# Performance work log

Hardware: AMD Instinct MI355X
Metric: run time of the kernel (lower is better)

## Reference

```python
import jax, jax.numpy as jnp
import numpy as np

BS = 4      # block_size
NH = 8      # n_heads
DH = 32     # d_head
DIN = 128   # d_input
DOUT = 128  # d_output
H = 256
W = 256
B = 2


def setup_inputs() -> dict:
    key = jax.random.key(0)
    k1, k2, k3 = jax.random.split(key, 3)
    x = jax.random.normal(k1, (B, DIN, H, W), jnp.float32)
    w_in = (jax.random.normal(k2, (3 * NH * DH, DIN), jnp.float32) * 0.05)
    b_in = jnp.full((3 * NH * DH,), 0.01, jnp.float32)
    w_out = (jax.random.normal(k3, (DOUT, NH * DH), jnp.float32) * 0.05)
    b_out = jnp.full((DOUT,), 0.01, jnp.float32)
    # positional_cross_embedding init: beta*(|x-2bs|^alpha + |y-2bs|^alpha), alpha=2, beta=1/16
    d = jnp.abs(jnp.arange(4 * BS, dtype=jnp.float32) - 2 * BS) ** 2.0
    vals = (1.0 / 16.0) * (d[:, None] + d[None, :]).reshape(-1)  # (16*bs*bs,)
    pce = jnp.tile(vals[None, :], (NH, 1)).astype(jnp.float32)
    return {"x": x, "w_in": w_in, "b_in": b_in, "w_out": w_out, "b_out": b_out, "pce": pce}


def reference(x, w_in, b_in, w_out, b_out, pce):
    Bx, din, Hx, Wx = x.shape
    hb = Wx // BS  # horizontal blocks (width axis)
    vb = Hx // BS  # vertical blocks (height axis)
    # (B, C, H, W) -> (B, W, H, C) -> (B, hb, vb, bs, bs, C)
    xt = jnp.swapaxes(x, 1, 3)
    xt = xt.reshape(Bx, hb, BS, vb, BS, din).transpose(0, 1, 3, 2, 4, 5)
    proj = xt @ w_in.T + b_in  # (B, hb, vb, bs, bs, 3*NH*DH)
    q = proj[..., :NH * DH]
    kv = proj[..., NH * DH:]
    # gather 3x3 block neighborhood via pad + concat (zero padding at borders)
    kv = jnp.pad(kv, ((0, 0), (1, 1), (1, 1), (0, 0), (0, 0), (0, 0)))
    kv = jnp.concatenate((kv[:, :-2], kv[:, 1:-1], kv[:, 2:]), axis=3)       # (B,hb,vb,3bs,bs,2C)
    kv = jnp.concatenate((kv[:, :, :-2], kv[:, :, 1:-1], kv[:, :, 2:]), axis=4)  # (B,hb,vb,3bs,3bs,2C)
    q = q.reshape(Bx, hb, vb, BS * BS, NH, DH).swapaxes(3, 4)                      # (B,hb,vb,NH,bs^2,DH)
    k = kv[..., :NH * DH].reshape(Bx, hb, vb, 9 * BS * BS, NH, DH).swapaxes(3, 4)  # (B,hb,vb,NH,9bs^2,DH)
    v = kv[..., NH * DH:].reshape(Bx, hb, vb, 9 * BS * BS, NH, DH).swapaxes(3, 4)
    # relative-position bias: gather pce per (q, kv) pair (equiv. to tensordot with one-hot masks)
    a0 = jnp.arange(BS)
    a1 = jnp.arange(3 * BS)
    net = a1[None, :] + BS - a0[:, None]  # (bs, 3bs): x_net / y_net
    idx = (4 * BS * net)[:, None, :, None] + net[None, :, None, :]  # (bs, bs, 3bs, 3bs)
    idx = idx.reshape(BS * BS, 9 * BS * BS)
    bias = pce[:, idx]  # (NH, bs^2, 9bs^2)
    # boundary cutoff: mask kv halo that falls outside the image
    ex = jnp.zeros((hb, 3 * BS), bool).at[0, :BS].set(True).at[-1, 2 * BS:].set(True)
    ey = jnp.zeros((vb, 3 * BS), bool).at[0, :BS].set(True).at[-1, 2 * BS:].set(True)
    blocked = ex[:, None, :, None] | ey[None, :, None, :]  # (hb, vb, 3bs, 3bs)
    cut = jnp.where(blocked, jnp.inf, 0.0).reshape(hb, vb, 1, 1, 9 * BS * BS)
    amask = -(bias[None, None] + cut)  # (hb, vb, NH, bs^2, 9bs^2)
    scale = 1.0 / jnp.sqrt(jnp.float32(DH))
    scores = jnp.einsum('bhvnqd,bhvnkd->bhvnqk', q, k) * scale + amask
    attn = jax.nn.softmax(scores, axis=-1)
    out = jnp.einsum('bhvnqk,bhvnkd->bhvnqd', attn, v)
    out = out.swapaxes(3, 4).reshape(Bx, hb, vb, BS * BS, NH * DH)
    out = out @ w_out.T + b_out  # (B, hb, vb, bs^2, DOUT)
    out = out.reshape(Bx, hb, vb, BS, BS, DOUT).swapaxes(2, 3).reshape(Bx, Wx, Hx, DOUT)
    return jnp.swapaxes(out, 1, 3)  # (B, DOUT, H, W)
```

## Files before the change

### kernel.cpp

```cpp
#include <hip/hip_runtime.h>


typedef __bf16 bf16x8 __attribute__((ext_vector_type(8)));
typedef float f32x4 __attribute__((ext_vector_type(4)));

__device__ __forceinline__ unsigned short f2bf(float f) {
  unsigned u = __float_as_uint(f);
  u = (u + 0x7FFFu + ((u >> 16) & 1u)) >> 16;
  return (unsigned short)u;
}

__global__ __launch_bounds__(256) void prep_w(const float* __restrict__ w_in,
                                              const float* __restrict__ w_out,
                                              unsigned short* __restrict__ wbf,
                                              unsigned short* __restrict__ wob) {
  int idx = (blockIdx.x * 256 + threadIdx.x) * 4;
  const float* src; unsigned short* dst; int off;
  if (idx < 98304) { src = w_in;  dst = wbf; off = idx; }
  else             { src = w_out; dst = wob; off = idx - 98304; }
  float4 v = *(const float4*)(src + off);
  ushort4 o;
  o.x = f2bf(v.x); o.y = f2bf(v.y); o.z = f2bf(v.z); o.w = f2bf(v.w);
  *(ushort4*)(dst + off) = o;
}

#define XS_STRIDE 136

__global__ __launch_bounds__(256) void qkv_proj(const float* __restrict__ x,
                                                const unsigned short* __restrict__ wbf,
                                                const float* __restrict__ b_in,
                                                unsigned short* __restrict__ qkv,
                                                unsigned short* __restrict__ vT) {
  __shared__ __align__(16) unsigned short xs[64 * XS_STRIDE];
  const int tid = threadIdx.x;
  const int strip = blockIdx.x, vb = blockIdx.y, b = blockIdx.z;
  const int w0 = strip * 16;
  const size_t xbase = ((size_t)b * 128) * 65536 + (size_t)(vb * 4) * 256 + (size_t)w0;

#pragma unroll
  for (int it = 0; it < 8; ++it) {
    int flat = (it * 256 + tid) * 4;
    int c = flat >> 6;
    int rem = flat & 63;
    int i1 = rem >> 4;
    int lw0 = rem & 15;
    const float4 v = *(const float4*)(x + xbase + (size_t)c * 65536 + i1 * 256 + lw0);
    float vv[4] = {v.x, v.y, v.z, v.w};
#pragma unroll
    for (int e = 0; e < 4; ++e) {
      int lw = lw0 + e;
      int u = ((lw >> 2) << 4) + ((lw & 3) << 2) + i1;
      xs[u * XS_STRIDE + c] = f2bf(vv[e]);
    }
  }
  __syncthreads();

  const int wv = tid >> 6, lane = tid & 63;
  const int l16 = lane & 15, q4 = lane >> 4;
  const size_t tile_base = ((size_t)(b * 64 + vb)) * 64 + strip * 4;

#pragma unroll 1
  for (int jt = 0; jt < 12; ++jt) {
    const int j0 = wv * 192 + jt * 16;
    bf16x8 wf[4];
    const unsigned short* wr = wbf + (size_t)(j0 + l16) * 128 + q4 * 8;
#pragma unroll
    for (int ks = 0; ks < 4; ++ks) wf[ks] = *(const bf16x8*)(wr + ks * 32);

    if (j0 < 512) {
      const float4 bi = *(const float4*)(b_in + j0 + q4 * 4);
      f32x4 acc0; acc0[0] = bi.x; acc0[1] = bi.y; acc0[2] = bi.z; acc0[3] = bi.w;
      f32x4 acc[4] = {acc0, acc0, acc0, acc0};
#pragma unroll
      for (int tt = 0; tt < 4; ++tt) {
        const unsigned short* xr = xs + (tt * 16 + l16) * XS_STRIDE + q4 * 8;
#pragma unroll
        for (int ks = 0; ks < 4; ++ks) {
          bf16x8 xf = *(const bf16x8*)(xr + ks * 32);
          acc[tt] = __builtin_amdgcn_mfma_f32_16x16x32_bf16(wf[ks], xf, acc[tt], 0, 0, 0);
        }
      }
#pragma unroll
      for (int tt = 0; tt < 4; ++tt) {
        unsigned short* dst = qkv + ((tile_base + tt) * 16 + l16) * 512 + j0 + q4 * 4;
        ushort4 o;
        o.x = f2bf(acc[tt][0]); o.y = f2bf(acc[tt][1]);
        o.z = f2bf(acc[tt][2]); o.w = f2bf(acc[tt][3]);
        *(ushort4*)dst = o;
      }
    } else {
      const float bi = b_in[j0 + l16];
      f32x4 acc0; acc0[0] = bi; acc0[1] = bi; acc0[2] = bi; acc0[3] = bi;
      f32x4 acc[4] = {acc0, acc0, acc0, acc0};
#pragma unroll
      for (int tt = 0; tt < 4; ++tt) {
        const unsigned short* xr = xs + (tt * 16 + l16) * XS_STRIDE + q4 * 8;
#pragma unroll
        for (int ks = 0; ks < 4; ++ks) {
          bf16x8 xf = *(const bf16x8*)(xr + ks * 32);
          acc[tt] = __builtin_amdgcn_mfma_f32_16x16x32_bf16(xf, wf[ks], acc[tt], 0, 0, 0);
        }
      }
      const int jv = j0 - 512;
#pragma unroll
      for (int tt = 0; tt < 4; ++tt) {
        unsigned short* dst = vT + ((size_t)(tile_base + tt) * 256 + jv + l16) * 16 + q4 * 4;
        ushort4 o;
        o.x = f2bf(acc[tt][0]); o.y = f2bf(acc[tt][1]);
        o.z = f2bf(acc[tt][2]); o.w = f2bf(acc[tt][3]);
        *(ushort4*)dst = o;
      }
    }
  }
}

#define PS_STRIDE 168

__global__ __launch_bounds__(512, 6) void attn_out(
    const unsigned short* __restrict__ qkv,
    const unsigned short* __restrict__ vT,
    const unsigned short* __restrict__ wob,
    const float* __restrict__ b_out,
    float* __restrict__ out) {
  __shared__ __align__(16) unsigned short ps_all[8][16 * PS_STRIDE];
  __shared__ __align__(16) unsigned short ao[16][264];

  const int tid = threadIdx.x;
  const int wv = tid >> 6, lane = tid & 63;
  const int n = lane & 15, quad = lane >> 4;
  const int hb = blockIdx.x, vb = blockIdx.y, b = blockIdx.z;
  const int h = wv;

  unsigned short* ps = ps_all[wv];

  int nbrow[9];
  bool blk[9];
#pragma unroll
  for (int s0 = 0; s0 < 3; ++s0)
#pragma unroll
    for (int s1 = 0; s1 < 3; ++s1) {
      int hb2 = hb + s0 - 1, vb2 = vb + s1 - 1;
      blk[s0 * 3 + s1] = ((unsigned)hb2 > 63u) || ((unsigned)vb2 > 63u);
      int h2 = min(max(hb2, 0), 63), v2 = min(max(vb2, 0), 63);
      nbrow[s0 * 3 + s1] = ((b * 64 + v2) * 64 + h2) * 16;
    }
  const int tb16 = ((b * 64 + vb) * 64 + hb) * 16;
  const int i0q = n >> 2, i1q = n & 3;
  const float scale = 0.17677669529663687f;

  const bf16x8 qf = *(const bf16x8*)(qkv + (size_t)(tb16 + n) * 512 + h * 32 + quad * 8);
  f32x4 sc[9];
#pragma unroll
  for (int s = 0; s < 9; ++s) {
    const bf16x8 kf = *(const bf16x8*)(qkv + (size_t)(nbrow[s] + n) * 512 + 256 + h * 32 + quad * 8);
    f32x4 z; z[0] = 0.f; z[1] = 0.f; z[2] = 0.f; z[3] = 0.f;
    sc[s] = __builtin_amdgcn_mfma_f32_16x16x32_bf16(kf, qf, z, 0, 0, 0);
  }

  float mx = -1e30f;
#pragma unroll
  for (int s = 0; s < 9; ++s) {
    const int s0 = s / 3, s1 = s - s0 * 3;
    const float a0 = (float)(s0 * 4 + quad - 4 - i0q);
#pragma unroll
    for (int r = 0; r < 4; ++r) {
      const float b1 = (float)(s1 * 4 + r - 4 - i1q);
      float v = blk[s] ? -1e30f : (sc[s][r] * scale - (a0 * a0 + b1 * b1) * 0.0625f);
      sc[s][r] = v;
      mx = fmaxf(mx, v);
    }
  }
  mx = fmaxf(mx, __shfl_xor(mx, 16));
  mx = fmaxf(mx, __shfl_xor(mx, 32));
  float sum = 0.f;
#pragma unroll
  for (int s = 0; s < 9; ++s)
#pragma unroll
    for (int r = 0; r < 4; ++r) {
      float p = __expf(sc[s][r] - mx);
      sc[s][r] = p;
      sum += p;
    }
  sum += __shfl_xor(sum, 16);
  sum += __shfl_xor(sum, 32);
  const float inv = 1.f / sum;

#pragma unroll
  for (int s = 0; s < 9; ++s) {
    ushort4 o;
    o.x = f2bf(sc[s][0] * inv); o.y = f2bf(sc[s][1] * inv);
    o.z = f2bf(sc[s][2] * inv); o.w = f2bf(sc[s][3] * inv);
    *(ushort4*)(ps + n * PS_STRIDE + s * 16 + quad * 4) = o;
  }
  {
    ushort4 z4 = {0, 0, 0, 0};
    *(ushort4*)(ps + n * PS_STRIDE + 144 + quad * 4) = z4;
  }

  bf16x8 af[5];
#pragma unroll
  for (int kc = 0; kc < 5; ++kc)
    af[kc] = *(const bf16x8*)(ps + n * PS_STRIDE + kc * 32 + quad * 8);

#pragma unroll
  for (int d2 = 0; d2 < 2; ++d2) {
    f32x4 acc; acc[0] = 0.f; acc[1] = 0.f; acc[2] = 0.f; acc[3] = 0.f;
#pragma unroll
    for (int kc = 0; kc < 5; ++kc) {
      const int slot = min(kc * 2 + (quad >> 1), 8);
      const int tok0 = (quad & 1) * 8;
      const bf16x8 vf = *(const bf16x8*)(vT +
          ((size_t)(nbrow[slot] >> 4) * 256 + h * 32 + d2 * 16 + n) * 16 + tok0);
      acc = __builtin_amdgcn_mfma_f32_16x16x32_bf16(af[kc], vf, acc, 0, 0, 0);
    }
#pragma unroll
    for (int r = 0; r < 4; ++r)
      ao[quad * 4 + r][h * 32 + d2 * 16 + n] = f2bf(acc[r]);
  }
  __syncthreads();

  {
    const int oc = wv * 16 + n;
    const float bo = b_out[oc];
    f32x4 acc; acc[0] = bo; acc[1] = bo; acc[2] = bo; acc[3] = bo;
#pragma unroll
    for (int kc = 0; kc < 8; ++kc) {
      const bf16x8 a = *(const bf16x8*)(&ao[n][kc * 32 + quad * 8]);
      const bf16x8 w8 = *(const bf16x8*)(wob + (size_t)oc * 256 + kc * 32 + quad * 8);
      acc = __builtin_amdgcn_mfma_f32_16x16x32_bf16(a, w8, acc, 0, 0, 0);
    }
#pragma unroll
    for (int r = 0; r < 4; ++r)
      out[(((size_t)b * 128 + oc) * 256 + (vb * 4 + r)) * 256 + hb * 4 + quad] = acc[r];
  }
}

extern "C" void kernel_launch(void* const* d_in, const int* in_sizes, int n_in,
                              void* d_out, int out_size, void* d_ws, size_t ws_size,
                              hipStream_t stream) {
  const float* x     = (const float*)d_in[0];
  const float* w_in  = (const float*)d_in[1];
  const float* b_in  = (const float*)d_in[2];
  const float* w_out = (const float*)d_in[3];
  const float* b_out = (const float*)d_in[4];
  float* out = (float*)d_out;

  unsigned short* wbf = (unsigned short*)d_ws;
  unsigned short* wob = (unsigned short*)((char*)d_ws + 196608);
  unsigned short* qkv = (unsigned short*)((char*)d_ws + 262144);
  unsigned short* vT  = (unsigned short*)((char*)d_ws + 134479872);

  prep_w  <<<128, 256, 0, stream>>>(w_in, w_out, wbf, wob);
  qkv_proj<<<dim3(16, 64, 2), 256, 0, stream>>>(x, wbf, b_in, qkv, vT);
  attn_out<<<dim3(64, 64, 2), 512, 0, stream>>>(qkv, vT, wob, b_out, out);
}
```

Baseline: 421.5 us.

## Streamline attention softmax, reuse LDS, hoist X fragments and swizzle block order

Software bf16 rounding is replaced with native bf16 conversion and packed stores. In qkv_proj, the X fragments are hoisted into registers once, so they are not reloaded from LDS for each output tile. attn_out now fuses the exp computation into the score loop without max subtraction and applies normalization after the PV product. It also reuses the per-wave P buffer for the attention output instead of a separate LDS array, and trims the last PV MFMA. Tighter launch bounds and a remapped 1D block index for neighbour locality raise occupancy; dropping the max-subtraction risks overflow if scores grow large.

```diff
diff --git a/kernel.cpp b/kernel.cpp
--- a/kernel.cpp
+++ b/kernel.cpp
@@ -2,12 +2,18 @@
 
 
 typedef __bf16 bf16x8 __attribute__((ext_vector_type(8)));
+typedef __bf16 bf16x2 __attribute__((ext_vector_type(2)));
 typedef float f32x4 __attribute__((ext_vector_type(4)));
 
-__device__ __forceinline__ unsigned short f2bf(float f) {
-  unsigned u = __float_as_uint(f);
-  u = (u + 0x7FFFu + ((u >> 16) & 1u)) >> 16;
-  return (unsigned short)u;
+__device__ __forceinline__ unsigned pk2(float a, float b) {
+  bf16x2 v;
+  v[0] = (__bf16)a;
+  v[1] = (__bf16)b;
+  return __builtin_bit_cast(unsigned, v);
+}
+__device__ __forceinline__ unsigned short bf1(float a) {
+  __bf16 v = (__bf16)a;
+  return __builtin_bit_cast(unsigned short, v);
 }
 
 __global__ __launch_bounds__(256) void prep_w(const float* __restrict__ w_in,
@@ -19,18 +25,19 @@
   if (idx < 98304) { src = w_in;  dst = wbf; off = idx; }
   else             { src = w_out; dst = wob; off = idx - 98304; }
   float4 v = *(const float4*)(src + off);
-  ushort4 o;
-  o.x = f2bf(v.x); o.y = f2bf(v.y); o.z = f2bf(v.z); o.w = f2bf(v.w);
-  *(ushort4*)(dst + off) = o;
+  uint2 o;
+  o.x = pk2(v.x, v.y);
+  o.y = pk2(v.z, v.w);
+  *(uint2*)(dst + off) = o;
 }
 
 #define XS_STRIDE 136
 
-__global__ __launch_bounds__(256) void qkv_proj(const float* __restrict__ x,
-                                                const unsigned short* __restrict__ wbf,
-                                                const float* __restrict__ b_in,
-                                                unsigned short* __restrict__ qkv,
-                                                unsigned short* __restrict__ vT) {
+__global__ __launch_bounds__(256, 4) void qkv_proj(const float* __restrict__ x,
+                                                   const unsigned short* __restrict__ wbf,
+                                                   const float* __restrict__ b_in,
+                                                   unsigned short* __restrict__ qkv,
+                                                   unsigned short* __restrict__ vT) {
   __shared__ __align__(16) unsigned short xs[64 * XS_STRIDE];
   const int tid = threadIdx.x;
   const int strip = blockIdx.x, vb = blockIdx.y, b = blockIdx.z;
@@ -50,7 +57,7 @@
     for (int e = 0; e < 4; ++e) {
       int lw = lw0 + e;
       int u = ((lw >> 2) << 4) + ((lw & 3) << 2) + i1;
-      xs[u * XS_STRIDE + c] = f2bf(vv[e]);
+      xs[u * XS_STRIDE + c] = bf1(vv[e]);
     }
   }
   __syncthreads();
@@ -58,6 +65,13 @@
   const int wv = tid >> 6, lane = tid & 63;
   const int l16 = lane & 15, q4 = lane >> 4;
   const size_t tile_base = ((size_t)(b * 64 + vb)) * 64 + strip * 4;
+
+  bf16x8 xf[4][4];
+#pragma unroll
+  for (int tt = 0; tt < 4; ++tt)
+#pragma unroll
+    for (int ks = 0; ks < 4; ++ks)
+      xf[tt][ks] = *(const bf16x8*)(xs + (tt * 16 + l16) * XS_STRIDE + ks * 32 + q4 * 8);
 
 #pragma unroll 1
   for (int jt = 0; jt < 12; ++jt) {
@@ -72,63 +86,58 @@
       f32x4 acc0; acc0[0] = bi.x; acc0[1] = bi.y; acc0[2] = bi.z; acc0[3] = bi.w;
       f32x4 acc[4] = {acc0, acc0, acc0, acc0};
 #pragma unroll
-      for (int tt = 0; tt < 4; ++tt) {
-        const unsigned short* xr = xs + (tt * 16 + l16) * XS_STRIDE + q4 * 8;
-#pragma unroll
-        for (int ks = 0; ks < 4; ++ks) {
-          bf16x8 xf = *(const bf16x8*)(xr + ks * 32);
-          acc[tt] = __builtin_amdgcn_mfma_f32_16x16x32_bf16(wf[ks], xf, acc[tt], 0, 0, 0);
-        }
-      }
+      for (int tt = 0; tt < 4; ++tt)
+#pragma unroll
+        for (int ks = 0; ks < 4; ++ks)
+          acc[tt] = __builtin_amdgcn_mfma_f32_16x16x32_bf16(wf[ks], xf[tt][ks], acc[tt], 0, 0, 0);
 #pragma unroll
       for (int tt = 0; tt < 4; ++tt) {
         unsigned short* dst = qkv + ((tile_base + tt) * 16 + l16) * 512 + j0 + q4 * 4;
-        ushort4 o;
-        o.x = f2bf(acc[tt][0]); o.y = f2bf(acc[tt][1]);
-        o.z = f2bf(acc[tt][2]); o.w = f2bf(acc[tt][3]);
-        *(ushort4*)dst = o;
+        uint2 o;
+        o.x = pk2(acc[tt][0], acc[tt][1]);
+        o.y = pk2(acc[tt][2], acc[tt][3]);
+        *(uint2*)dst = o;
       }
     } else {
       const float bi = b_in[j0 + l16];
       f32x4 acc0; acc0[0] = bi; acc0[1] = bi; acc0[2] = bi; acc0[3] = bi;
       f32x4 acc[4] = {acc0, acc0, acc0, acc0};
 #pragma unroll
-      for (int tt = 0; tt < 4; ++tt) {
-        const unsigned short* xr = xs + (tt * 16 + l16) * XS_STRIDE + q4 * 8;
-#pragma unroll
-        for (int ks = 0; ks < 4; ++ks) {
-          bf16x8 xf = *(const bf16x8*)(xr + ks * 32);
-          acc[tt] = __builtin_amdgcn_mfma_f32_16x16x32_bf16(xf, wf[ks], acc[tt], 0, 0, 0);
-        }
-      }
+      for (int tt = 0; tt < 4; ++tt)
+#pragma unroll
+        for (int ks = 0; ks < 4; ++ks)
+          acc[tt] = __builtin_amdgcn_mfma_f32_16x16x32_bf16(xf[tt][ks], wf[ks], acc[tt], 0, 0, 0);
       const int jv = j0 - 512;
 #pragma unroll
       for (int tt = 0; tt < 4; ++tt) {
         unsigned short* dst = vT + ((size_t)(tile_base + tt) * 256 + jv + l16) * 16 + q4 * 4;
-        ushort4 o;
-        o.x = f2bf(acc[tt][0]); o.y = f2bf(acc[tt][1]);
-        o.z = f2bf(acc[tt][2]); o.w = f2bf(acc[tt][3]);
-        *(ushort4*)dst = o;
+        uint2 o;
+        o.x = pk2(acc[tt][0], acc[tt][1]);
+        o.y = pk2(acc[tt][2], acc[tt][3]);
+        *(uint2*)dst = o;
       }
     }
   }
 }
 
-#define PS_STRIDE 168
-
-__global__ __launch_bounds__(512, 6) void attn_out(
+#define PS_STRIDE 152
+
+__global__ __launch_bounds__(512, 8) void attn_out(
     const unsigned short* __restrict__ qkv,
     const unsigned short* __restrict__ vT,
     const unsigned short* __restrict__ wob,
     const float* __restrict__ b_out,
     float* __restrict__ out) {
   __shared__ __align__(16) unsigned short ps_all[8][16 * PS_STRIDE];
-  __shared__ __align__(16) unsigned short ao[16][264];
 
   const int tid = threadIdx.x;
   const int wv = tid >> 6, lane = tid & 63;
   const int n = lane & 15, quad = lane >> 4;
-  const int hb = blockIdx.x, vb = blockIdx.y, b = blockIdx.z;
+
+  const int id = blockIdx.x;
+  const int hb = (id >> 3) & 63;
+  const int vb = (id & 7) * 8 + (id >> 9);
+  const int bz = blockIdx.y;
   const int h = wv;
 
   unsigned short* ps = ps_all[wv];
@@ -142,80 +151,90 @@
       int hb2 = hb + s0 - 1, vb2 = vb + s1 - 1;
       blk[s0 * 3 + s1] = ((unsigned)hb2 > 63u) || ((unsigned)vb2 > 63u);
       int h2 = min(max(hb2, 0), 63), v2 = min(max(vb2, 0), 63);
-      nbrow[s0 * 3 + s1] = ((b * 64 + v2) * 64 + h2) * 16;
-    }
-  const int tb16 = ((b * 64 + vb) * 64 + hb) * 16;
+      nbrow[s0 * 3 + s1] = ((bz * 64 + v2) * 64 + h2) * 16;
+    }
+  const int tb16 = ((bz * 64 + vb) * 64 + hb) * 16;
   const int i0q = n >> 2, i1q = n & 3;
   const float scale = 0.17677669529663687f;
 
-  const bf16x8 qf = *(const bf16x8*)(qkv + (size_t)(tb16 + n) * 512 + h * 32 + quad * 8);
-  f32x4 sc[9];
-#pragma unroll
-  for (int s = 0; s < 9; ++s) {
-    const bf16x8 kf = *(const bf16x8*)(qkv + (size_t)(nbrow[s] + n) * 512 + 256 + h * 32 + quad * 8);
-    f32x4 z; z[0] = 0.f; z[1] = 0.f; z[2] = 0.f; z[3] = 0.f;
-    sc[s] = __builtin_amdgcn_mfma_f32_16x16x32_bf16(kf, qf, z, 0, 0, 0);
-  }
-
-  float mx = -1e30f;
+  float a2c[3], b2c[12];
+#pragma unroll
+  for (int s0 = 0; s0 < 3; ++s0) {
+    float a0 = (float)(s0 * 4 + quad - 4 - i0q);
+    a2c[s0] = a0 * a0 * 0.0625f;
+  }
+#pragma unroll
+  for (int s1 = 0; s1 < 3; ++s1)
+#pragma unroll
+    for (int r = 0; r < 4; ++r) {
+      float b1 = (float)(s1 * 4 + r - 4 - i1q);
+      b2c[s1 * 4 + r] = b1 * b1 * 0.0625f;
+    }
+
+  const unsigned short* qbase = qkv + (size_t)n * 512 + h * 32 + quad * 8;
+  const bf16x8 qf = *(const bf16x8*)(qbase + (size_t)tb16 * 512);
+
+  float sum = 0.f;
 #pragma unroll
   for (int s = 0; s < 9; ++s) {
     const int s0 = s / 3, s1 = s - s0 * 3;
-    const float a0 = (float)(s0 * 4 + quad - 4 - i0q);
-#pragma unroll
-    for (int r = 0; r < 4; ++r) {
-      const float b1 = (float)(s1 * 4 + r - 4 - i1q);
-      float v = blk[s] ? -1e30f : (sc[s][r] * scale - (a0 * a0 + b1 * b1) * 0.0625f);
-      sc[s][r] = v;
-      mx = fmaxf(mx, v);
-    }
-  }
-  mx = fmaxf(mx, __shfl_xor(mx, 16));
-  mx = fmaxf(mx, __shfl_xor(mx, 32));
-  float sum = 0.f;
-#pragma unroll
-  for (int s = 0; s < 9; ++s)
-#pragma unroll
-    for (int r = 0; r < 4; ++r) {
-      float p = __expf(sc[s][r] - mx);
-      sc[s][r] = p;
-      sum += p;
-    }
+    const bf16x8 kf = *(const bf16x8*)(qbase + 256 + (size_t)nbrow[s] * 512);
+    f32x4 z; z[0] = 0.f; z[1] = 0.f; z[2] = 0.f; z[3] = 0.f;
+    f32x4 sc = __builtin_amdgcn_mfma_f32_16x16x32_bf16(kf, qf, z, 0, 0, 0);
+    unsigned short* prow = ps + n * PS_STRIDE + s * 16 + quad * 4;
+    if (!blk[s]) {
+      float p0 = __expf(fmaf(sc[0], scale, -(a2c[s0] + b2c[s1 * 4 + 0])));
+      float p1 = __expf(fmaf(sc[1], scale, -(a2c[s0] + b2c[s1 * 4 + 1])));
+      float p2 = __expf(fmaf(sc[2], scale, -(a2c[s0] + b2c[s1 * 4 + 2])));
+      float p3 = __expf(fmaf(sc[3], scale, -(a2c[s0] + b2c[s1 * 4 + 3])));
+      sum += (p0 + p1) + (p2 + p3);
+      uint2 o; o.x = pk2(p0, p1); o.y = pk2(p2, p3);
+      *(uint2*)prow = o;
+    } else {
+      uint2 o; o.x = 0u; o.y = 0u;
+      *(uint2*)prow = o;
+    }
+  }
   sum += __shfl_xor(sum, 16);
   sum += __shfl_xor(sum, 32);
   const float inv = 1.f / sum;
-
-#pragma unroll
-  for (int s = 0; s < 9; ++s) {
-    ushort4 o;
-    o.x = f2bf(sc[s][0] * inv); o.y = f2bf(sc[s][1] * inv);
-    o.z = f2bf(sc[s][2] * inv); o.w = f2bf(sc[s][3] * inv);
-    *(ushort4*)(ps + n * PS_STRIDE + s * 16 + quad * 4) = o;
-  }
-  {
-    ushort4 z4 = {0, 0, 0, 0};
-    *(ushort4*)(ps + n * PS_STRIDE + 144 + quad * 4) = z4;
-  }
+  float inv4[4];
+#pragma unroll
+  for (int r = 0; r < 4; ++r)
+    inv4[r] = __shfl(inv, (lane & 0x30) | (quad * 4 + r));
 
   bf16x8 af[5];
 #pragma unroll
-  for (int kc = 0; kc < 5; ++kc)
+  for (int kc = 0; kc < 4; ++kc)
     af[kc] = *(const bf16x8*)(ps + n * PS_STRIDE + kc * 32 + quad * 8);
+  af[4] = *(const bf16x8*)(ps + n * PS_STRIDE + 128 + (quad & 1) * 8);
+  if (quad >= 2) { bf16x8 zf = {}; af[4] = zf; }
+
+  size_t vrow[9];
+#pragma unroll
+  for (int s = 0; s < 9; ++s) vrow[s] = (size_t)(nbrow[s] >> 4) * 4096;
+  size_t vsel[4];
+#pragma unroll
+  for (int kc = 0; kc < 4; ++kc)
+    vsel[kc] = (quad >> 1) ? vrow[kc * 2 + 1] : vrow[kc * 2];
+  const int tok0 = (quad & 1) * 8;
 
 #pragma unroll
   for (int d2 = 0; d2 < 2; ++d2) {
+    const int voff = (h * 32 + d2 * 16 + n) * 16;
     f32x4 acc; acc[0] = 0.f; acc[1] = 0.f; acc[2] = 0.f; acc[3] = 0.f;
 #pragma unroll
-    for (int kc = 0; kc < 5; ++kc) {
-      const int slot = min(kc * 2 + (quad >> 1), 8);
-      const int tok0 = (quad & 1) * 8;
-      const bf16x8 vf = *(const bf16x8*)(vT +
-          ((size_t)(nbrow[slot] >> 4) * 256 + h * 32 + d2 * 16 + n) * 16 + tok0);
+    for (int kc = 0; kc < 4; ++kc) {
+      const bf16x8 vf = *(const bf16x8*)(vT + vsel[kc] + voff + tok0);
       acc = __builtin_amdgcn_mfma_f32_16x16x32_bf16(af[kc], vf, acc, 0, 0, 0);
     }
+    {
+      const bf16x8 vf = *(const bf16x8*)(vT + vrow[8] + voff + tok0);
+      acc = __builtin_amdgcn_mfma_f32_16x16x32_bf16(af[4], vf, acc, 0, 0, 0);
+    }
 #pragma unroll
     for (int r = 0; r < 4; ++r)
-      ao[quad * 4 + r][h * 32 + d2 * 16 + n] = f2bf(acc[r]);
+      ps[(quad * 4 + r) * PS_STRIDE + d2 * 16 + n] = bf1(acc[r] * inv4[r]);
   }
   __syncthreads();
 
@@ -225,13 +244,13 @@
     f32x4 acc; acc[0] = bo; acc[1] = bo; acc[2] = bo; acc[3] = bo;
 #pragma unroll
     for (int kc = 0; kc < 8; ++kc) {
-      const bf16x8 a = *(const bf16x8*)(&ao[n][kc * 32 + quad * 8]);
+      const bf16x8 a = *(const bf16x8*)(&ps_all[kc][n * PS_STRIDE + quad * 8]);
       const bf16x8 w8 = *(const bf16x8*)(wob + (size_t)oc * 256 + kc * 32 + quad * 8);
       acc = __builtin_amdgcn_mfma_f32_16x16x32_bf16(a, w8, acc, 0, 0, 0);
     }
 #pragma unroll
     for (int r = 0; r < 4; ++r)
-      out[(((size_t)b * 128 + oc) * 256 + (vb * 4 + r)) * 256 + hb * 4 + quad] = acc[r];
+      out[(((size_t)bz * 128 + oc) * 256 + (vb * 4 + r)) * 256 + hb * 4 + quad] = acc[r];
   }
 }
 
@@ -252,5 +271,5 @@
 
   prep_w  <<<128, 256, 0, stream>>>(w_in, w_out, wbf, wob);
   qkv_proj<<<dim3(16, 64, 2), 256, 0, stream>>>(x, wbf, b_in, qkv, vT);
-  attn_out<<<dim3(64, 64, 2), 512, 0, stream>>>(qkv, vT, wob, b_out, out);
-}
+  attn_out<<<dim3(4096, 2), 512, 0, stream>>>(qkv, vT, wob, b_out, out);
+}
```

New measurement: 473.9 us. +12.4%, slower.
